# Performance work log

Measured on AMD Instinct MI355X. Metric: run time of the kernel, lower is better.

Reference implementation:

```python
import jax, jax.numpy as jnp
import numpy as np

HID = 256
NUM_ENT = 100000
NUM_REL = 50
E = 320000  # edges per direction; edge_index has 2*E columns
BN_EPS = 1e-5


def setup_inputs() -> dict:
    key = jax.random.key(0)
    ks = jax.random.split(key, 10)
    x = jax.random.normal(ks[0], (NUM_ENT, HID), dtype=jnp.float32)
    edge_index = jax.random.randint(ks[1], (2, 2 * E), 0, NUM_ENT)
    edge_type = jax.random.randint(ks[2], (2 * E,), 0, NUM_REL)
    rel_embed = jax.random.normal(ks[3], (NUM_REL, HID), dtype=jnp.float32)
    # xavier_normal init: std = sqrt(2 / (fan_in + fan_out))
    w_std = (2.0 / (HID + HID)) ** 0.5
    w_loop = jax.random.normal(ks[4], (HID, HID), dtype=jnp.float32) * w_std
    w_in = jax.random.normal(ks[5], (HID, HID), dtype=jnp.float32) * w_std
    w_out = jax.random.normal(ks[6], (HID, HID), dtype=jnp.float32) * w_std
    w_rel = jax.random.normal(ks[7], (HID, HID), dtype=jnp.float32) * w_std
    loop_rel = jax.random.normal(ks[8], (1, HID), dtype=jnp.float32) * ((2.0 / (1 + HID)) ** 0.5)
    bn_weight = jnp.ones((HID,), dtype=jnp.float32)
    bn_bias = jnp.zeros((HID,), dtype=jnp.float32)
    return {
        "x": x, "edge_index": edge_index, "edge_type": edge_type,
        "rel_embed": rel_embed, "w_loop": w_loop, "w_in": w_in,
        "w_out": w_out, "w_rel": w_rel, "loop_rel": loop_rel,
        "bn_weight": bn_weight, "bn_bias": bn_bias,
    }


def _compute_norm(edge_index, num_ent):
    # symmetric D^-1/2 * D^-1/2 norm; degree counted on row (target) index
    row, col = edge_index[0], edge_index[1]
    deg = jax.ops.segment_sum(jnp.ones_like(row, dtype=jnp.float32), row, num_segments=num_ent)
    deg_inv = jnp.where(deg > 0, deg ** -0.5, 0.0)
    return deg_inv[row] * deg_inv[col]


def _propagate(x, idx, etype, rel_all, W, norm, num_ent):
    # gather source nodes (idx[1]), compose with relation emb (mult), transform, scale, scatter-add to targets (idx[0])
    msg = (x[idx[1]] * rel_all[etype]) @ W  # [E, d]
    if norm is not None:
        msg = msg * norm[:, None]
    return jax.ops.segment_sum(msg, idx[0], num_segments=num_ent)


def reference(x, edge_index, edge_type, rel_embed, w_loop, w_in, w_out, w_rel,
              loop_rel, bn_weight, bn_bias):
    num_ent = x.shape[0]
    rel_all = jnp.concatenate([rel_embed, loop_rel], axis=0)  # [R+1, d]
    e = edge_index.shape[1] // 2
    in_index, out_index = edge_index[:, :e], edge_index[:, e:]
    in_type, out_type = edge_type[:e], edge_type[e:]

    in_norm = _compute_norm(in_index, num_ent)
    out_norm = _compute_norm(out_index, num_ent)

    in_res = _propagate(x, in_index, in_type, rel_all, w_in, in_norm, num_ent)
    out_res = _propagate(x, out_index, out_type, rel_all, w_out, out_norm, num_ent)
    # self-loop: identity scatter -> just per-node compose+transform
    loop_res = (x * loop_rel) @ w_loop

    out = (in_res + out_res + loop_res) * (1.0 / 3.0)

    # BatchNorm1d in training mode (batch stats, biased variance)
    mean = out.mean(axis=0)
    var = out.var(axis=0)
    out = (out - mean) * jax.lax.rsqrt(var + BN_EPS) * bn_weight + bn_bias

    rel_out = (rel_all @ w_rel)[:-1]  # drop loop relation
    return out, rel_out
```

## Files before the change

### kernel.cpp

```cpp
#include <hip/hip_runtime.h>

#define HID     256
#define N_ENT   100000
#define TOT_E   640000
#define HALF_E  320000
#define NSEG    (2 * N_ENT)
#define BN_EPSF 1e-5f
#define SCAN_ELEMS 1024
#define NBLK_SCAN  ((NSEG + SCAN_ELEMS - 1) / SCAN_ELEMS)

typedef short bf16x8 __attribute__((ext_vector_type(8)));
typedef float f32x4  __attribute__((ext_vector_type(4)));

__device__ __forceinline__ short f2b(float f) {
    union { float f; unsigned u; } c; c.f = f;
    unsigned u = c.u;
    u += 0x7FFF + ((u >> 16) & 1);
    return (short)(u >> 16);
}
__device__ __forceinline__ float b2f(short b) {
    union { unsigned u; float f; } c;
    c.u = ((unsigned)(unsigned short)b) << 16;
    return c.f;
}
__device__ __forceinline__ void gload16(const void* g, void* l) {
    __builtin_amdgcn_global_load_lds(
        (const __attribute__((address_space(1))) unsigned*)(g),
        (__attribute__((address_space(3))) unsigned*)(l), 16, 0, 0);
}

__global__ void hist_kernel(const int* __restrict__ ei, int* __restrict__ offs) {
    int j = blockIdx.x * 256 + threadIdx.x;
    if (j >= TOT_E) return;
    int seg = ei[j] + ((j < HALF_E) ? 0 : N_ENT);
    atomicAdd(&offs[seg], 1);
}

__global__ __launch_bounds__(256) void scan1(int* __restrict__ offs, int* __restrict__ bsums,
                                             float* __restrict__ rnorm) {
    __shared__ int tsum[256];
    int b = blockIdx.x, t = threadIdx.x;
    int base = b * SCAN_ELEMS + t * 4;
    int v[4] = {0, 0, 0, 0};
    if (base + 3 < NSEG) {
        int4 lv = *(const int4*)(offs + base);
        v[0] = lv.x; v[1] = lv.y; v[2] = lv.z; v[3] = lv.w;
    } else {
        for (int i = 0; i < 4; ++i) if (base + i < NSEG) v[i] = offs[base + i];
    }
    #pragma unroll
    for (int i = 0; i < 4; ++i)
        if (base + i < NSEG)
            rnorm[base + i] = (v[i] > 0) ? rsqrtf((float)v[i]) : 0.f;
    tsum[t] = v[0] + v[1] + v[2] + v[3];
    __syncthreads();
    for (int d = 1; d < 256; d <<= 1) {
        int val = (t >= d) ? tsum[t - d] : 0;
        __syncthreads();
        tsum[t] += val;
        __syncthreads();
    }
    int run = (t == 0) ? 0 : tsum[t - 1];
    if (t == 255) bsums[b] = tsum[255];
    int w[4];
    for (int i = 0; i < 4; ++i) { w[i] = run; run += v[i]; }
    if (base + 3 < NSEG) *(int4*)(offs + base) = make_int4(w[0], w[1], w[2], w[3]);
    else for (int i = 0; i < 4; ++i) if (base + i < NSEG) offs[base + i] = w[i];
}

__global__ __launch_bounds__(256) void scan3f(int* __restrict__ offs, const int* __restrict__ bsums) {
    __shared__ int tmp[256];
    int b = blockIdx.x, t = threadIdx.x;
    tmp[t] = (t < NBLK_SCAN) ? bsums[t] : 0;
    __syncthreads();
    for (int d = 1; d < 256; d <<= 1) {
        int val = (t >= d) ? tmp[t - d] : 0;
        __syncthreads();
        tmp[t] += val;
        __syncthreads();
    }
    int add = (b == 0) ? 0 : tmp[b - 1];
    int base = b * SCAN_ELEMS + t * 4;
    if (base + 3 < NSEG) {
        int4 v = *(int4*)(offs + base);
        v.x += add; v.y += add; v.z += add; v.w += add;
        *(int4*)(offs + base) = v;
    } else {
        for (int i = 0; i < 4; ++i) if (base + i < NSEG) offs[base + i] += add;
    }
}

__global__ void fill8_kernel(const int* __restrict__ ei, const int* __restrict__ et,
                             int* __restrict__ offs, const float* __restrict__ rnorm,
                             int2* __restrict__ elist8) {
    int j = blockIdx.x * 256 + threadIdx.x;
    if (j >= TOT_E) return;
    int hb  = (j < HALF_E) ? 0 : N_ENT;
    int seg = ei[j] + hb;
    int col = ei[TOT_E + j];
    float norm = rnorm[seg] * rnorm[hb + col];
    int pos = atomicAdd(&offs[seg], 1);
    elist8[pos] = make_int2(col | (et[j] << 17), __float_as_int(norm));
}

#define NX8 (N_ENT * HID / 8)
#define NR8 (50 * HID / 8)
__global__ void tobf16_both(const float* __restrict__ x, short* __restrict__ xh,
                            const float* __restrict__ rel, short* __restrict__ relh) {
    int i = blockIdx.x * 256 + threadIdx.x;
    const float* src; short* dst; int idx;
    if (i < NX8) { src = x; dst = xh; idx = i; }
    else if (i < NX8 + NR8) { src = rel; dst = relh; idx = i - NX8; }
    else return;
    const float4* p = (const float4*)(src + (size_t)idx * 8);
    float4 v0 = p[0], v1 = p[1];
    bf16x8 pk;
    pk[0]=f2b(v0.x); pk[1]=f2b(v0.y); pk[2]=f2b(v0.z); pk[3]=f2b(v0.w);
    pk[4]=f2b(v1.x); pk[5]=f2b(v1.y); pk[6]=f2b(v1.z); pk[7]=f2b(v1.w);
    *(bf16x8*)(dst + (size_t)idx * 8) = pk;
}

__global__ __launch_bounds__(256) void gather_h(
        const short* __restrict__ xh, const short* __restrict__ relh,
        const int* __restrict__ offs, const int2* __restrict__ elist8,
        short* __restrict__ accA, short* __restrict__ accB) {
    int s = blockIdx.x * 8 + (threadIdx.x >> 5);
    int lane = threadIdx.x & 31;
    int start = (s == 0) ? 0 : offs[s - 1];
    int end   = offs[s];
    float a0[8], a1[8], a2[8], a3[8];
    #pragma unroll
    for (int k = 0; k < 8; ++k) { a0[k]=0.f; a1[k]=0.f; a2[k]=0.f; a3[k]=0.f; }
    int e = start;
    for (; e + 4 <= end; e += 4) {
        int2 p0 = elist8[e], p1 = elist8[e+1], p2 = elist8[e+2], p3 = elist8[e+3];
        int c0 = p0.x & 0x1FFFF, t0 = p0.x >> 17; float n0 = __int_as_float(p0.y);
        int c1 = p1.x & 0x1FFFF, t1 = p1.x >> 17; float n1 = __int_as_float(p1.y);
        int c2 = p2.x & 0x1FFFF, t2 = p2.x >> 17; float n2 = __int_as_float(p2.y);
        int c3 = p3.x & 0x1FFFF, t3 = p3.x >> 17; float n3 = __int_as_float(p3.y);
        bf16x8 xv0 = *(const bf16x8*)(xh + (size_t)c0 * HID + lane * 8);
        bf16x8 xv1 = *(const bf16x8*)(xh + (size_t)c1 * HID + lane * 8);
        bf16x8 xv2 = *(const bf16x8*)(xh + (size_t)c2 * HID + lane * 8);
        bf16x8 xv3 = *(const bf16x8*)(xh + (size_t)c3 * HID + lane * 8);
        bf16x8 rv0 = *(const bf16x8*)(relh + (size_t)t0 * HID + lane * 8);
        bf16x8 rv1 = *(const bf16x8*)(relh + (size_t)t1 * HID + lane * 8);
        bf16x8 rv2 = *(const bf16x8*)(relh + (size_t)t2 * HID + lane * 8);
        bf16x8 rv3 = *(const bf16x8*)(relh + (size_t)t3 * HID + lane * 8);
        #pragma unroll
        for (int k = 0; k < 8; ++k) {
            a0[k] += b2f(xv0[k]) * b2f(rv0[k]) * n0;
            a1[k] += b2f(xv1[k]) * b2f(rv1[k]) * n1;
            a2[k] += b2f(xv2[k]) * b2f(rv2[k]) * n2;
            a3[k] += b2f(xv3[k]) * b2f(rv3[k]) * n3;
        }
    }
    for (; e < end; ++e) {
        int2 p = elist8[e];
        int c = p.x & 0x1FFFF, t = p.x >> 17;
        float n = __int_as_float(p.y);
        bf16x8 xv = *(const bf16x8*)(xh   + (size_t)c * HID + lane * 8);
        bf16x8 rv = *(const bf16x8*)(relh + (size_t)t * HID + lane * 8);
        #pragma unroll
        for (int k = 0; k < 8; ++k)
            a0[k] += b2f(xv[k]) * b2f(rv[k]) * n;
    }
    int hb = (s >= N_ENT) ? N_ENT : 0;
    short* dst = ((s >= N_ENT) ? accB : accA) + (size_t)(s - hb) * HID + lane * 8;
    bf16x8 pk;
    #pragma unroll
    for (int k = 0; k < 8; ++k) pk[k] = f2b((a0[k] + a1[k]) + (a2[k] + a3[k]));
    *(bf16x8*)dst = pk;
}

__global__ void wcat_kernel(const float* __restrict__ w_in, const float* __restrict__ w_out,
                            const float* __restrict__ w_loop, const float* __restrict__ loop_rel,
                            short* __restrict__ WT) {
    int n = blockIdx.x;
    int t = threadIdx.x;
    float v0 = w_in  [(size_t)t * HID + n];
    float v1 = w_out [(size_t)t * HID + n];
    float v2 = w_loop[(size_t)t * HID + n] * loop_rel[t];
    short* row = WT + (size_t)n * 768;
    row[t]       = f2b(v0);
    row[256 + t] = f2b(v1);
    row[512 + t] = f2b(v2);
}

template <bool BF16OUT>
__global__ __launch_bounds__(256) void gemm_mfma_db32(
        const short* __restrict__ accA, const short* __restrict__ accB,
        const short* __restrict__ xh, const short* __restrict__ WT,
        float* __restrict__ out, short* __restrict__ outh, float* __restrict__ stats)
{
    __shared__ __align__(16) short As[2][64 * 32];
    __shared__ __align__(16) short Bs[2][256 * 32];
    const int tid = threadIdx.x;
    const int l   = tid & 63;
    const int wid = tid >> 6;
    const int r0  = blockIdx.x * 64;
    const int lr  = l & 15;
    const int lg  = l >> 4;

    f32x4 acc[4][4];
    #pragma unroll
    for (int i = 0; i < 4; ++i)
        #pragma unroll
        for (int j = 0; j < 4; ++j)
            acc[i][j] = (f32x4){0.f, 0.f, 0.f, 0.f};

    auto stage = [&](int buf, int kt) {
        const int src = kt >> 3;
        const short* Ap = (src == 0) ? accA : ((src == 1) ? accB : xh);
        const int ksl = (kt & 7) * 32;
        const int ksg = kt * 32;
        {
            int r  = wid * 16 + (l >> 2);
            int sg = (l & 3) ^ (r & 3);
            int gr = r0 + r;
            if (gr >= N_ENT) gr = N_ENT - 1;
            gload16(Ap + (size_t)gr * HID + ksl + sg * 8, &As[buf][wid * 512]);
        }
        #pragma unroll
        for (int i = 0; i < 4; ++i) {
            int n  = wid * 64 + i * 16 + (l >> 2);
            int sg = (l & 3) ^ (n & 3);
            gload16(WT + (size_t)n * 768 + ksg + sg * 8, &Bs[buf][wid * 2048 + i * 512]);
        }
    };

    stage(0, 0);
    __syncthreads();
    int cur = 0;
    for (int kt = 0; kt < 24; ++kt) {
        if (kt < 23) stage(cur ^ 1, kt + 1);
        bf16x8 af[4], bfr[4];
        #pragma unroll
        for (int i = 0; i < 4; ++i) {
            int r = 16 * i + lr;
            af[i] = *(const bf16x8*)&As[cur][r * 32 + ((lg ^ (r & 3)) << 3)];
        }
        #pragma unroll
        for (int j = 0; j < 4; ++j) {
            int n = wid * 64 + 16 * j + lr;
            bfr[j] = *(const bf16x8*)&Bs[cur][n * 32 + ((lg ^ (n & 3)) << 3)];
        }
        #pragma unroll
        for (int i = 0; i < 4; ++i)
            #pragma unroll
            for (int j = 0; j < 4; ++j)
                acc[i][j] = __builtin_amdgcn_mfma_f32_16x16x32_bf16(
                                af[i], bfr[j], acc[i][j], 0, 0, 0);
        __syncthreads();
        cur ^= 1;
    }

    const float third = 1.f / 3.f;
    float s[4]  = {0.f, 0.f, 0.f, 0.f};
    float sq[4] = {0.f, 0.f, 0.f, 0.f};
    #pragma unroll
    for (int i = 0; i < 4; ++i) {
        #pragma unroll
        for (int v = 0; v < 4; ++v) {
            int grow = r0 + 16 * i + lg * 4 + v;
            if (grow < N_ENT) {
                #pragma unroll
                for (int j = 0; j < 4; ++j) {
                    float val = acc[i][j][v] * third;
                    int col = wid * 64 + 16 * j + lr;
                    if (BF16OUT) outh[(size_t)grow * HID + col] = f2b(val);
                    else         out [(size_t)grow * HID + col] = val;
                    s[j] += val; sq[j] += val * val;
                }
            }
        }
    }
    #pragma unroll
    for (int j = 0; j < 4; ++j) {
        s[j]  += __shfl_xor(s[j], 16);  s[j]  += __shfl_xor(s[j], 32);
        sq[j] += __shfl_xor(sq[j], 16); sq[j] += __shfl_xor(sq[j], 32);
    }
    if (lg == 0) {
        #pragma unroll
        for (int j = 0; j < 4; ++j) {
            int c = wid * 64 + 16 * j + lr;
            atomicAdd(&stats[c], s[j]);
            atomicAdd(&stats[HID + c], sq[j]);
        }
    }
}

__global__ void bn_apply_h(const short* __restrict__ outh, float* __restrict__ out,
                           const float* __restrict__ stats,
                           const float* __restrict__ bnw, const float* __restrict__ bnb) {
    const float invN = 1.f / (float)N_ENT;
    const int total8 = N_ENT * (HID / 8);
    for (int i = blockIdx.x * 256 + threadIdx.x; i < total8; i += gridDim.x * 256) {
        int c = (i & 31) * 8;
        bf16x8 v = *(const bf16x8*)(outh + (size_t)i * 8);
        float r[8];
        #pragma unroll
        for (int k = 0; k < 8; ++k) {
            float mean = stats[c + k] * invN;
            float var  = stats[HID + c + k] * invN - mean * mean;
            float sc   = rsqrtf(var + BN_EPSF) * bnw[c + k];
            float sh   = bnb[c + k] - mean * sc;
            r[k] = b2f(v[k]) * sc + sh;
        }
        float4* dst = (float4*)(out + (size_t)i * 8);
        dst[0] = make_float4(r[0], r[1], r[2], r[3]);
        dst[1] = make_float4(r[4], r[5], r[6], r[7]);
    }
}

__global__ void bn_apply(float* __restrict__ out, const float* __restrict__ stats,
                         const float* __restrict__ bnw, const float* __restrict__ bnb) {
    const float invN = 1.f / (float)N_ENT;
    const int total4 = N_ENT * (HID / 4);
    for (int i = blockIdx.x * 256 + threadIdx.x; i < total4; i += gridDim.x * 256) {
        int c = (i & 63) * 4;
        float4 v = *(float4*)(out + (size_t)i * 4);
        #pragma unroll
        for (int k = 0; k < 4; ++k) {
            float mean = stats[c + k] * invN;
            float var  = stats[HID + c + k] * invN - mean * mean;
            float sc   = rsqrtf(var + BN_EPSF) * bnw[c + k];
            float sh   = bnb[c + k] - mean * sc;
            float* comp = (k == 0) ? &v.x : (k == 1) ? &v.y : (k == 2) ? &v.z : &v.w;
            *comp = (*comp) * sc + sh;
        }
        *(float4*)(out + (size_t)i * 4) = v;
    }
}

__global__ void relout_kernel(const float* __restrict__ rel_embed,
                              const float* __restrict__ w_rel,
                              float* __restrict__ rel_out) {
    __shared__ float row[HID];
    int r = blockIdx.x;
    int c = threadIdx.x;
    row[c] = rel_embed[(size_t)r * HID + c];
    __syncthreads();
    float s = 0.f;
    #pragma unroll 8
    for (int k = 0; k < HID; ++k) s += row[k] * w_rel[(size_t)k * HID + c];
    rel_out[(size_t)r * HID + c] = s;
}

extern "C" void kernel_launch(void* const* d_in, const int* in_sizes, int n_in,
                              void* d_out, int out_size, void* d_ws, size_t ws_size,
                              hipStream_t stream) {
    const float* x        = (const float*)d_in[0];
    const int*   ei       = (const int*)d_in[1];
    const int*   et       = (const int*)d_in[2];
    const float* rel      = (const float*)d_in[3];
    const float* w_loop   = (const float*)d_in[4];
    const float* w_in     = (const float*)d_in[5];
    const float* w_out    = (const float*)d_in[6];
    const float* w_rel    = (const float*)d_in[7];
    const float* loop_rel = (const float*)d_in[8];
    const float* bnw      = (const float*)d_in[9];
    const float* bnb      = (const float*)d_in[10];

    float* out     = (float*)d_out;
    float* rel_out = out + (size_t)N_ENT * HID;

    const size_t XH_B   = (size_t)N_ENT * HID * 2;
    const size_t ACC_B  = (size_t)N_ENT * HID * 2;
    const size_t OFFS_B = (size_t)NSEG * 4;
    const size_t EL8_B  = (size_t)TOT_E * 8;
    const size_t RN_B   = (size_t)NSEG * 4;
    const size_t RELH_B = (size_t)50 * HID * 2;
    const size_t base_need = XH_B + 2 * ACC_B + OFFS_B + EL8_B + RN_B
                           + 256 * 4 + 512 * 4 + RELH_B;
    const size_t OUTH_B = (size_t)N_ENT * HID * 2;
    const bool   have_outh = (ws_size >= base_need + OUTH_B);

    char* w = (char*)d_ws;
    short* xh     = (short*)w;              w += XH_B;
    short* accA_h = (short*)w;              w += ACC_B;
    short* accB_h = (short*)w;              w += ACC_B;
    int*   offs   = (int*)w;                w += OFFS_B;
    int2*  elist8 = (int2*)w;               short* WT = (short*)w;   w += EL8_B;
    float* rnorm  = (float*)w;              w += RN_B;
    int*   bsums  = (int*)w;                w += 256 * 4;
    float* stats  = (float*)w;              w += 512 * 4;
    short* relh   = (short*)w;              w += RELH_B;
    short* outh   = (short*)w;

    hipMemsetAsync(offs, 0, OFFS_B, stream);
    hipMemsetAsync(stats, 0, 512 * 4, stream);

    tobf16_both<<<(NX8 + NR8 + 255) / 256, 256, 0, stream>>>(x, xh, rel, relh);
    hist_kernel<<<TOT_E / 256, 256, 0, stream>>>(ei, offs);
    scan1<<<NBLK_SCAN, 256, 0, stream>>>(offs, bsums, rnorm);
    scan3f<<<NBLK_SCAN, 256, 0, stream>>>(offs, bsums);
    fill8_kernel<<<TOT_E / 256, 256, 0, stream>>>(ei, et, offs, rnorm, elist8);
    gather_h<<<NSEG / 8, 256, 0, stream>>>(xh, relh, offs, elist8, accA_h, accB_h);
    wcat_kernel<<<256, 256, 0, stream>>>(w_in, w_out, w_loop, loop_rel, WT);
    if (have_outh) {
        gemm_mfma_db32<true><<<(N_ENT + 63) / 64, 256, 0, stream>>>(
            accA_h, accB_h, xh, WT, out, outh, stats);
        bn_apply_h<<<1024, 256, 0, stream>>>(outh, out, stats, bnw, bnb);
    } else {
        gemm_mfma_db32<false><<<(N_ENT + 63) / 64, 256, 0, stream>>>(
            accA_h, accB_h, xh, WT, out, outh, stats);
        bn_apply<<<1024, 256, 0, stream>>>(out, stats, bnw, bnb);
    }
    relout_kernel<<<50, 256, 0, stream>>>(rel, w_rel, rel_out);
}
```

Measured before the change: 354.9 us.

## Retile GEMM to 128-row single-buffered K64 tiles and widen gather to wave-per-segment

The GEMM now computes 128 rows per block with 64-wide K tiles, loaded through registers with an 8-way XOR swizzle. This replaces the 64-row double-buffered async global-to-LDS pipeline and is meant to halve the B-tile reloads per row and cut the number of barriers. The gather kernel now gives each segment a full 64-lane wave reading 4 bf16 per lane with 2-way unrolling, instead of a half-wave reading 8 per lane with 4-way unrolling. The cost is losing the load/compute overlap in the GEMM, plus fewer loads in flight per lane in the gather.

```diff
diff --git a/kernel.cpp b/kernel.cpp
--- a/kernel.cpp
+++ b/kernel.cpp
@@ -10,6 +10,7 @@
 #define NBLK_SCAN  ((NSEG + SCAN_ELEMS - 1) / SCAN_ELEMS)
 
 typedef short bf16x8 __attribute__((ext_vector_type(8)));
+typedef short bf16x4 __attribute__((ext_vector_type(4)));
 typedef float f32x4  __attribute__((ext_vector_type(4)));
 
 __device__ __forceinline__ short f2b(float f) {
@@ -22,11 +23,6 @@
     union { unsigned u; float f; } c;
     c.u = ((unsigned)(unsigned short)b) << 16;
     return c.f;
-}
-__device__ __forceinline__ void gload16(const void* g, void* l) {
-    __builtin_amdgcn_global_load_lds(
-        (const __attribute__((address_space(1))) unsigned*)(g),
-        (__attribute__((address_space(3))) unsigned*)(l), 16, 0, 0);
 }
 
 __global__ void hist_kernel(const int* __restrict__ ei, int* __restrict__ offs) {
@@ -124,52 +120,50 @@
         const short* __restrict__ xh, const short* __restrict__ relh,
         const int* __restrict__ offs, const int2* __restrict__ elist8,
         short* __restrict__ accA, short* __restrict__ accB) {
-    int s = blockIdx.x * 8 + (threadIdx.x >> 5);
-    int lane = threadIdx.x & 31;
+    int s = blockIdx.x * 4 + (threadIdx.x >> 6);
+    int lane = threadIdx.x & 63;
     int start = (s == 0) ? 0 : offs[s - 1];
     int end   = offs[s];
-    float a0[8], a1[8], a2[8], a3[8];
-    #pragma unroll
-    for (int k = 0; k < 8; ++k) { a0[k]=0.f; a1[k]=0.f; a2[k]=0.f; a3[k]=0.f; }
+    float ax0=0.f, ay0=0.f, az0=0.f, aw0=0.f;
+    float ax1=0.f, ay1=0.f, az1=0.f, aw1=0.f;
     int e = start;
-    for (; e + 4 <= end; e += 4) {
-        int2 p0 = elist8[e], p1 = elist8[e+1], p2 = elist8[e+2], p3 = elist8[e+3];
-        int c0 = p0.x & 0x1FFFF, t0 = p0.x >> 17; float n0 = __int_as_float(p0.y);
-        int c1 = p1.x & 0x1FFFF, t1 = p1.x >> 17; float n1 = __int_as_float(p1.y);
-        int c2 = p2.x & 0x1FFFF, t2 = p2.x >> 17; float n2 = __int_as_float(p2.y);
-        int c3 = p3.x & 0x1FFFF, t3 = p3.x >> 17; float n3 = __int_as_float(p3.y);
-        bf16x8 xv0 = *(const bf16x8*)(xh + (size_t)c0 * HID + lane * 8);
-        bf16x8 xv1 = *(const bf16x8*)(xh + (size_t)c1 * HID + lane * 8);
-        bf16x8 xv2 = *(const bf16x8*)(xh + (size_t)c2 * HID + lane * 8);
-        bf16x8 xv3 = *(const bf16x8*)(xh + (size_t)c3 * HID + lane * 8);
-        bf16x8 rv0 = *(const bf16x8*)(relh + (size_t)t0 * HID + lane * 8);
-        bf16x8 rv1 = *(const bf16x8*)(relh + (size_t)t1 * HID + lane * 8);
-        bf16x8 rv2 = *(const bf16x8*)(relh + (size_t)t2 * HID + lane * 8);
-        bf16x8 rv3 = *(const bf16x8*)(relh + (size_t)t3 * HID + lane * 8);
-        #pragma unroll
-        for (int k = 0; k < 8; ++k) {
-            a0[k] += b2f(xv0[k]) * b2f(rv0[k]) * n0;
-            a1[k] += b2f(xv1[k]) * b2f(rv1[k]) * n1;
-            a2[k] += b2f(xv2[k]) * b2f(rv2[k]) * n2;
-            a3[k] += b2f(xv3[k]) * b2f(rv3[k]) * n3;
-        }
-    }
-    for (; e < end; ++e) {
+    for (; e + 2 <= end; e += 2) {
+        int2 p0 = elist8[e];
+        int2 p1 = elist8[e + 1];
+        int   c0 = p0.x & 0x1FFFF, t0 = p0.x >> 17;
+        float n0 = __int_as_float(p0.y);
+        int   c1 = p1.x & 0x1FFFF, t1 = p1.x >> 17;
+        float n1 = __int_as_float(p1.y);
+        bf16x4 xv0 = *(const bf16x4*)(xh   + (size_t)c0 * HID + lane * 4);
+        bf16x4 rv0 = *(const bf16x4*)(relh + (size_t)t0 * HID + lane * 4);
+        bf16x4 xv1 = *(const bf16x4*)(xh   + (size_t)c1 * HID + lane * 4);
+        bf16x4 rv1 = *(const bf16x4*)(relh + (size_t)t1 * HID + lane * 4);
+        ax0 += b2f(xv0[0]) * b2f(rv0[0]) * n0;
+        ay0 += b2f(xv0[1]) * b2f(rv0[1]) * n0;
+        az0 += b2f(xv0[2]) * b2f(rv0[2]) * n0;
+        aw0 += b2f(xv0[3]) * b2f(rv0[3]) * n0;
+        ax1 += b2f(xv1[0]) * b2f(rv1[0]) * n1;
+        ay1 += b2f(xv1[1]) * b2f(rv1[1]) * n1;
+        az1 += b2f(xv1[2]) * b2f(rv1[2]) * n1;
+        aw1 += b2f(xv1[3]) * b2f(rv1[3]) * n1;
+    }
+    if (e < end) {
         int2 p = elist8[e];
-        int c = p.x & 0x1FFFF, t = p.x >> 17;
+        int   c = p.x & 0x1FFFF, t = p.x >> 17;
         float n = __int_as_float(p.y);
-        bf16x8 xv = *(const bf16x8*)(xh   + (size_t)c * HID + lane * 8);
-        bf16x8 rv = *(const bf16x8*)(relh + (size_t)t * HID + lane * 8);
-        #pragma unroll
-        for (int k = 0; k < 8; ++k)
-            a0[k] += b2f(xv[k]) * b2f(rv[k]) * n;
+        bf16x4 xv = *(const bf16x4*)(xh   + (size_t)c * HID + lane * 4);
+        bf16x4 rv = *(const bf16x4*)(relh + (size_t)t * HID + lane * 4);
+        ax0 += b2f(xv[0]) * b2f(rv[0]) * n;
+        ay0 += b2f(xv[1]) * b2f(rv[1]) * n;
+        az0 += b2f(xv[2]) * b2f(rv[2]) * n;
+        aw0 += b2f(xv[3]) * b2f(rv[3]) * n;
     }
     int hb = (s >= N_ENT) ? N_ENT : 0;
-    short* dst = ((s >= N_ENT) ? accB : accA) + (size_t)(s - hb) * HID + lane * 8;
-    bf16x8 pk;
-    #pragma unroll
-    for (int k = 0; k < 8; ++k) pk[k] = f2b((a0[k] + a1[k]) + (a2[k] + a3[k]));
-    *(bf16x8*)dst = pk;
+    short* dst = ((s >= N_ENT) ? accB : accA) + (size_t)(s - hb) * HID + lane * 4;
+    bf16x4 pk;
+    pk[0] = f2b(ax0 + ax1); pk[1] = f2b(ay0 + ay1);
+    pk[2] = f2b(az0 + az1); pk[3] = f2b(aw0 + aw1);
+    *(bf16x4*)dst = pk;
 }
 
 __global__ void wcat_kernel(const float* __restrict__ w_in, const float* __restrict__ w_out,
@@ -187,78 +181,77 @@
 }
 
 template <bool BF16OUT>
-__global__ __launch_bounds__(256) void gemm_mfma_db32(
+__global__ __launch_bounds__(256, 2) void gemm_mfma_128(
         const short* __restrict__ accA, const short* __restrict__ accB,
         const short* __restrict__ xh, const short* __restrict__ WT,
         float* __restrict__ out, short* __restrict__ outh, float* __restrict__ stats)
 {
-    __shared__ __align__(16) short As[2][64 * 32];
-    __shared__ __align__(16) short Bs[2][256 * 32];
+    __shared__ __align__(16) short As[128 * 64];
+    __shared__ __align__(16) short Bs[256 * 64];
     const int tid = threadIdx.x;
     const int l   = tid & 63;
     const int wid = tid >> 6;
-    const int r0  = blockIdx.x * 64;
+    const int r0  = blockIdx.x * 128;
     const int lr  = l & 15;
     const int lg  = l >> 4;
 
-    f32x4 acc[4][4];
+    f32x4 acc[8][4];
     #pragma unroll
-    for (int i = 0; i < 4; ++i)
+    for (int i = 0; i < 8; ++i)
         #pragma unroll
         for (int j = 0; j < 4; ++j)
             acc[i][j] = (f32x4){0.f, 0.f, 0.f, 0.f};
 
-    auto stage = [&](int buf, int kt) {
-        const int src = kt >> 3;
+    const int sg = tid & 7;
+    const int sr = tid >> 3;
+
+    for (int kt = 0; kt < 12; ++kt) {
+        const int src = kt >> 2;
         const short* Ap = (src == 0) ? accA : ((src == 1) ? accB : xh);
-        const int ksl = (kt & 7) * 32;
-        const int ksg = kt * 32;
-        {
-            int r  = wid * 16 + (l >> 2);
-            int sg = (l & 3) ^ (r & 3);
+        const int ksg = kt * 64;
+        const int ksl = (kt & 3) * 64;
+        __syncthreads();
+        #pragma unroll
+        for (int h = 0; h < 4; ++h) {
+            int r  = sr + 32 * h;
             int gr = r0 + r;
-            if (gr >= N_ENT) gr = N_ENT - 1;
-            gload16(Ap + (size_t)gr * HID + ksl + sg * 8, &As[buf][wid * 512]);
-        }
-        #pragma unroll
-        for (int i = 0; i < 4; ++i) {
-            int n  = wid * 64 + i * 16 + (l >> 2);
-            int sg = (l & 3) ^ (n & 3);
-            gload16(WT + (size_t)n * 768 + ksg + sg * 8, &Bs[buf][wid * 2048 + i * 512]);
-        }
-    };
-
-    stage(0, 0);
-    __syncthreads();
-    int cur = 0;
-    for (int kt = 0; kt < 24; ++kt) {
-        if (kt < 23) stage(cur ^ 1, kt + 1);
-        bf16x8 af[4], bfr[4];
-        #pragma unroll
-        for (int i = 0; i < 4; ++i) {
-            int r = 16 * i + lr;
-            af[i] = *(const bf16x8*)&As[cur][r * 32 + ((lg ^ (r & 3)) << 3)];
-        }
-        #pragma unroll
-        for (int j = 0; j < 4; ++j) {
-            int n = wid * 64 + 16 * j + lr;
-            bfr[j] = *(const bf16x8*)&Bs[cur][n * 32 + ((lg ^ (n & 3)) << 3)];
-        }
-        #pragma unroll
-        for (int i = 0; i < 4; ++i)
+            bf16x8 v = {0,0,0,0,0,0,0,0};
+            if (gr < N_ENT) v = *(const bf16x8*)(Ap + (size_t)gr * HID + ksl + sg * 8);
+            *(bf16x8*)&As[r * 64 + ((sg ^ (r & 7)) << 3)] = v;
+        }
+        #pragma unroll
+        for (int i = 0; i < 8; ++i) {
+            int n = sr + 32 * i;
+            bf16x8 w = *(const bf16x8*)(WT + (size_t)n * 768 + ksg + sg * 8);
+            *(bf16x8*)&Bs[n * 64 + ((sg ^ (n & 7)) << 3)] = w;
+        }
+        __syncthreads();
+        #pragma unroll
+        for (int kc = 0; kc < 2; ++kc) {
+            const int gsel = kc * 4 + lg;
+            bf16x8 bfr[4];
             #pragma unroll
-            for (int j = 0; j < 4; ++j)
-                acc[i][j] = __builtin_amdgcn_mfma_f32_16x16x32_bf16(
-                                af[i], bfr[j], acc[i][j], 0, 0, 0);
-        __syncthreads();
-        cur ^= 1;
+            for (int j = 0; j < 4; ++j) {
+                int n = wid * 64 + 16 * j + lr;
+                bfr[j] = *(const bf16x8*)&Bs[n * 64 + ((gsel ^ (n & 7)) << 3)];
+            }
+            #pragma unroll
+            for (int i = 0; i < 8; ++i) {
+                int r = 16 * i + lr;
+                bf16x8 af = *(const bf16x8*)&As[r * 64 + ((gsel ^ (r & 7)) << 3)];
+                #pragma unroll
+                for (int j = 0; j < 4; ++j)
+                    acc[i][j] = __builtin_amdgcn_mfma_f32_16x16x32_bf16(
+                                    af, bfr[j], acc[i][j], 0, 0, 0);
+            }
+        }
     }
 
     const float third = 1.f / 3.f;
     float s[4]  = {0.f, 0.f, 0.f, 0.f};
     float sq[4] = {0.f, 0.f, 0.f, 0.f};
     #pragma unroll
-    for (int i = 0; i < 4; ++i) {
+    for (int i = 0; i < 8; ++i) {
         #pragma unroll
         for (int v = 0; v < 4; ++v) {
             int grow = r0 + 16 * i + lg * 4 + v;
@@ -395,14 +388,14 @@
     scan1<<<NBLK_SCAN, 256, 0, stream>>>(offs, bsums, rnorm);
     scan3f<<<NBLK_SCAN, 256, 0, stream>>>(offs, bsums);
     fill8_kernel<<<TOT_E / 256, 256, 0, stream>>>(ei, et, offs, rnorm, elist8);
-    gather_h<<<NSEG / 8, 256, 0, stream>>>(xh, relh, offs, elist8, accA_h, accB_h);
+    gather_h<<<NSEG / 4, 256, 0, stream>>>(xh, relh, offs, elist8, accA_h, accB_h);
     wcat_kernel<<<256, 256, 0, stream>>>(w_in, w_out, w_loop, loop_rel, WT);
     if (have_outh) {
-        gemm_mfma_db32<true><<<(N_ENT + 63) / 64, 256, 0, stream>>>(
+        gemm_mfma_128<true><<<(N_ENT + 127) / 128, 256, 0, stream>>>(
             accA_h, accB_h, xh, WT, out, outh, stats);
         bn_apply_h<<<1024, 256, 0, stream>>>(outh, out, stats, bnw, bnb);
     } else {
-        gemm_mfma_db32<false><<<(N_ENT + 63) / 64, 256, 0, stream>>>(
+        gemm_mfma_128<false><<<(N_ENT + 127) / 128, 256, 0, stream>>>(
             accA_h, accB_h, xh, WT, out, outh, stats);
         bn_apply<<<1024, 256, 0, stream>>>(out, stats, bnw, bnb);
     }
```

Result: faster. 321.7 us (-9.4%).
